# Kernel tuning notes

Hardware: AMD Instinct MI355X
Metric: run time of the kernel (lower is better)

The kernel has to match this reference:

```python
import jax, jax.numpy as jnp
import numpy as np

NUM_HEADS = 8
LN_EPS = 1e-5


def setup_inputs() -> dict:
    key = jax.random.key(0)
    ks = jax.random.split(key, 9)
    B, C, H, W, T = 16, 512, 64, 64, 768
    x = jax.random.normal(ks[0], (B, C, H, W), dtype=jnp.float32)
    text_emb = jax.random.normal(ks[1], (B, T), dtype=jnp.float32)
    # nn.Linear weights are stored (out_features, in_features); y = x @ W.T
    Wq = jax.random.normal(ks[2], (C, C), dtype=jnp.float32) / np.sqrt(C)
    Wk = jax.random.normal(ks[3], (C, T), dtype=jnp.float32) / np.sqrt(T)
    Wv = jax.random.normal(ks[4], (C, T), dtype=jnp.float32) / np.sqrt(T)
    Wo = jax.random.normal(ks[5], (C, C), dtype=jnp.float32) / np.sqrt(C)
    bo = jax.random.normal(ks[6], (C,), dtype=jnp.float32) * 0.02
    gamma = jnp.ones((C,), dtype=jnp.float32)
    beta = jnp.zeros((C,), dtype=jnp.float32)
    return {"x": x, "text_emb": text_emb, "Wq": Wq, "Wk": Wk, "Wv": Wv,
            "Wo": Wo, "bo": bo, "gamma": gamma, "beta": beta}


def _layer_norm(h, gamma, beta):
    mu = jnp.mean(h, axis=-1, keepdims=True)
    var = jnp.mean(jnp.square(h - mu), axis=-1, keepdims=True)
    return (h - mu) * jax.lax.rsqrt(var + LN_EPS) * gamma + beta


def reference(x, text_emb, Wq, Wk, Wv, Wo, bo, gamma, beta):
    B, C, H, W = x.shape
    nh = NUM_HEADS
    hd = C // nh
    S = H * W
    # (B, S, C) spatial-token layout
    xr = x.reshape(B, C, S).transpose(0, 2, 1)
    q = (xr @ Wq.T).reshape(B, S, nh, hd).transpose(0, 2, 1, 3)      # (B, nh, S, hd)
    k = (text_emb @ Wk.T).reshape(B, 1, nh, hd).transpose(0, 2, 1, 3)  # (B, nh, 1, hd)
    v = (text_emb @ Wv.T).reshape(B, 1, nh, hd).transpose(0, 2, 1, 3)  # (B, nh, 1, hd)
    scale = hd ** (-0.5)
    scores = jnp.einsum('bnsh,bnkh->bnsk', q, k) * scale              # (B, nh, S, 1)
    attn = jax.nn.softmax(scores, axis=-1)                            # == 1.0 (single kv)
    out = jnp.einsum('bnsk,bnkh->bnsh', attn, v)                      # (B, nh, S, hd)
    out = out.transpose(0, 2, 1, 3).reshape(B, S, C)
    out = out @ Wo.T + bo
    y = _layer_norm(xr + out, gamma, beta)                            # (B, S, C)
    return y.transpose(0, 2, 1).reshape(B, C, H, W)
```

## Files before the change

### kernel.cpp

```cpp
#include <hip/hip_runtime.h>


constexpr int B = 16, C = 512, T = 768, S = 4096;
constexpr int TS = 32;
constexpr int BLK = 256;
constexpr float LN_EPS = 1e-5f;

template <int K, bool HAS_BIAS>
__global__ __launch_bounds__(256) void gemv_wave(const float* __restrict__ in,
                                                 const float* __restrict__ Wt,
                                                 const float* __restrict__ bias,
                                                 float* __restrict__ out) {
    const int w    = blockIdx.x * 4 + (threadIdx.x >> 6);
    const int lane = threadIdx.x & 63;
    const int b    = w >> 9;
    const int c    = w & (C - 1);
    const float4* wr = reinterpret_cast<const float4*>(Wt + (size_t)c * K);
    const float4* xr = reinterpret_cast<const float4*>(in + (size_t)b * K);
    float acc = 0.f;
#pragma unroll
    for (int i = lane; i < K / 4; i += 64) {
        float4 a = wr[i], t = xr[i];
        acc += a.x * t.x + a.y * t.y + a.z * t.z + a.w * t.w;
    }
#pragma unroll
    for (int off = 32; off > 0; off >>= 1) acc += __shfl_down(acc, off);
    if (lane == 0) out[b * C + c] = HAS_BIAS ? acc + bias[c] : acc;
}

__global__ __launch_bounds__(BLK) void fused_ln(const float* __restrict__ x,
                                                const float* __restrict__ a,
                                                const float* __restrict__ gamma,
                                                const float* __restrict__ beta,
                                                float* __restrict__ out) {
    __shared__ float tile[C * TS];
    __shared__ float a_s[C], g_s[C], be_s[C];
    __shared__ float psum[8 * TS], psq[8 * TS];
    __shared__ float mean_s[TS], rstd_s[TS];

    const int bid = blockIdx.x;
    const int b   = bid >> 7;
    const int s0  = (bid & 127) << 5;
    const int tid = threadIdx.x;

    for (int c = tid; c < C; c += BLK) {
        a_s[c]  = a[b * C + c];
        g_s[c]  = gamma[c];
        be_s[c] = beta[c];
    }

    const float* xb = x + (size_t)b * C * S + s0;
#pragma unroll
    for (int j = 0; j < 16; ++j) {
        int idx = j * BLK + tid;
        int c   = idx >> 3;
        int p   = (idx & 7) << 2;
        float4 v = *reinterpret_cast<const float4*>(xb + (size_t)c * S + p);
        *reinterpret_cast<float4*>(tile + c * TS + p) = v;
    }
    __syncthreads();

    const int w    = tid >> 6;
    const int l    = tid & 63;
    const int s    = l & 31;
    const int sub  = l >> 5;
    const int cbase = w * 128 + sub * 64;

    float sum = 0.f, sq = 0.f;
#pragma unroll 4
    for (int i = 0; i < 64; ++i) {
        int c = cbase + i;
        float v = tile[c * TS + s] + a_s[c];
        sum += v; sq += v * v;
    }
    psum[(w * 2 + sub) * TS + s] = sum;
    psq [(w * 2 + sub) * TS + s] = sq;
    __syncthreads();

    if (tid < TS) {
        float tsum = 0.f, tsq = 0.f;
#pragma unroll
        for (int j = 0; j < 8; ++j) { tsum += psum[j * TS + tid]; tsq += psq[j * TS + tid]; }
        float mu  = tsum * (1.f / C);
        float var = tsq * (1.f / C) - mu * mu;
        mean_s[tid] = mu;
        rstd_s[tid] = rsqrtf(var + LN_EPS);
    }
    __syncthreads();

    float* ob = out + (size_t)b * C * S + s0;
    const float mu = mean_s[s];
    const float rs = rstd_s[s];
#pragma unroll 4
    for (int i = 0; i < 64; ++i) {
        int c = cbase + i;
        float v = tile[c * TS + s] + a_s[c];
        ob[(size_t)c * S + s] = (v - mu) * rs * g_s[c] + be_s[c];
    }
}

extern "C" void kernel_launch(void* const* d_in, const int* in_sizes, int n_in,
                              void* d_out, int out_size, void* d_ws, size_t ws_size,
                              hipStream_t stream) {
    const float* x     = (const float*)d_in[0];
    const float* te    = (const float*)d_in[1];
    const float* Wv    = (const float*)d_in[4];
    const float* Wo    = (const float*)d_in[5];
    const float* bo    = (const float*)d_in[6];
    const float* gamma = (const float*)d_in[7];
    const float* beta  = (const float*)d_in[8];
    float* out = (float*)d_out;
    float* v   = (float*)d_ws;
    float* a   = (float*)d_ws + B * C;

    gemv_wave<T, false><<<B * C / 4, 256, 0, stream>>>(te, Wv, nullptr, v);
    gemv_wave<C, true ><<<B * C / 4, 256, 0, stream>>>(v,  Wo, bo,      a);
    fused_ln<<<B * (S / TS), BLK, 0, stream>>>(x, a, gamma, beta, out);
}
```

Before: 59.08 us.

## Keep LayerNorm tile in registers with float4 column-wise access and shuffle reductions

The fused LayerNorm kernel drops its 64KB shared-memory tile. Each block now covers 16 spatial positions with 512 threads. Every thread holds four float4 values of x in registers, reduces sums across channels with xor shuffles plus a small cross-wave shared-memory step, and writes the result back with vectorized stores. This cuts shared-memory traffic and LDS footprint, which should raise occupancy and allow float4 stores. The cost is short 64-byte contiguous segments per channel row, which may hurt memory coalescing.

```diff
diff --git a/kernel.cpp b/kernel.cpp
--- a/kernel.cpp
+++ b/kernel.cpp
@@ -2,8 +2,6 @@
 
 
 constexpr int B = 16, C = 512, T = 768, S = 4096;
-constexpr int TS = 32;
-constexpr int BLK = 256;
 constexpr float LN_EPS = 1e-5f;
 
 template <int K, bool HAS_BIAS>
@@ -28,74 +26,80 @@
     if (lane == 0) out[b * C + c] = HAS_BIAS ? acc + bias[c] : acc;
 }
 
-__global__ __launch_bounds__(BLK) void fused_ln(const float* __restrict__ x,
+__global__ __launch_bounds__(512) void fused_ln(const float* __restrict__ x,
                                                 const float* __restrict__ a,
                                                 const float* __restrict__ gamma,
                                                 const float* __restrict__ beta,
                                                 float* __restrict__ out) {
-    __shared__ float tile[C * TS];
     __shared__ float a_s[C], g_s[C], be_s[C];
-    __shared__ float psum[8 * TS], psq[8 * TS];
-    __shared__ float mean_s[TS], rstd_s[TS];
+    __shared__ float4 ps[32], pq[32];
 
     const int bid = blockIdx.x;
-    const int b   = bid >> 7;
-    const int s0  = (bid & 127) << 5;
-    const int tid = threadIdx.x;
+    const int b   = bid >> 8;
+    const int s0  = (bid & 255) << 4;
+    const int t   = threadIdx.x;
+    const int s4  = t & 3;
+    const int m   = t >> 2;
 
-    for (int c = tid; c < C; c += BLK) {
-        a_s[c]  = a[b * C + c];
-        g_s[c]  = gamma[c];
-        be_s[c] = beta[c];
+    const float4* xb4 = reinterpret_cast<const float4*>(x + (size_t)b * C * S + s0);
+    float4 xv[4];
+#pragma unroll
+    for (int i = 0; i < 4; ++i)
+        xv[i] = xb4[(size_t)(m + 128 * i) * (S / 4) + s4];
+
+    a_s[t]  = a[b * C + t];
+    g_s[t]  = gamma[t];
+    be_s[t] = beta[t];
+    __syncthreads();
+
+    float4 sum4 = {0.f, 0.f, 0.f, 0.f}, sq4 = {0.f, 0.f, 0.f, 0.f};
+#pragma unroll
+    for (int i = 0; i < 4; ++i) {
+        const float ac = a_s[m + 128 * i];
+        xv[i].x += ac; xv[i].y += ac; xv[i].z += ac; xv[i].w += ac;
+        sum4.x += xv[i].x; sum4.y += xv[i].y; sum4.z += xv[i].z; sum4.w += xv[i].w;
+        sq4.x  += xv[i].x * xv[i].x; sq4.y += xv[i].y * xv[i].y;
+        sq4.z  += xv[i].z * xv[i].z; sq4.w += xv[i].w * xv[i].w;
     }
 
-    const float* xb = x + (size_t)b * C * S + s0;
 #pragma unroll
-    for (int j = 0; j < 16; ++j) {
-        int idx = j * BLK + tid;
-        int c   = idx >> 3;
-        int p   = (idx & 7) << 2;
-        float4 v = *reinterpret_cast<const float4*>(xb + (size_t)c * S + p);
-        *reinterpret_cast<float4*>(tile + c * TS + p) = v;
+    for (int mask = 4; mask <= 32; mask <<= 1) {
+        sum4.x += __shfl_xor(sum4.x, mask); sum4.y += __shfl_xor(sum4.y, mask);
+        sum4.z += __shfl_xor(sum4.z, mask); sum4.w += __shfl_xor(sum4.w, mask);
+        sq4.x  += __shfl_xor(sq4.x,  mask); sq4.y  += __shfl_xor(sq4.y,  mask);
+        sq4.z  += __shfl_xor(sq4.z,  mask); sq4.w  += __shfl_xor(sq4.w,  mask);
     }
+    const int w = t >> 6, l = t & 63;
+    if (l < 4) { ps[w * 4 + l] = sum4; pq[w * 4 + l] = sq4; }
     __syncthreads();
 
-    const int w    = tid >> 6;
-    const int l    = tid & 63;
-    const int s    = l & 31;
-    const int sub  = l >> 5;
-    const int cbase = w * 128 + sub * 64;
+    float4 tot = {0.f, 0.f, 0.f, 0.f}, tq = {0.f, 0.f, 0.f, 0.f};
+#pragma unroll
+    for (int wv = 0; wv < 8; ++wv) {
+        float4 p = ps[wv * 4 + s4];
+        float4 q = pq[wv * 4 + s4];
+        tot.x += p.x; tot.y += p.y; tot.z += p.z; tot.w += p.w;
+        tq.x  += q.x; tq.y  += q.y; tq.z  += q.z; tq.w  += q.w;
+    }
+    constexpr float inv = 1.f / C;
+    float4 mu, rs;
+    mu.x = tot.x * inv; mu.y = tot.y * inv; mu.z = tot.z * inv; mu.w = tot.w * inv;
+    rs.x = rsqrtf(tq.x * inv - mu.x * mu.x + LN_EPS);
+    rs.y = rsqrtf(tq.y * inv - mu.y * mu.y + LN_EPS);
+    rs.z = rsqrtf(tq.z * inv - mu.z * mu.z + LN_EPS);
+    rs.w = rsqrtf(tq.w * inv - mu.w * mu.w + LN_EPS);
 
-    float sum = 0.f, sq = 0.f;
-#pragma unroll 4
-    for (int i = 0; i < 64; ++i) {
-        int c = cbase + i;
-        float v = tile[c * TS + s] + a_s[c];
-        sum += v; sq += v * v;
-    }
-    psum[(w * 2 + sub) * TS + s] = sum;
-    psq [(w * 2 + sub) * TS + s] = sq;
-    __syncthreads();
-
-    if (tid < TS) {
-        float tsum = 0.f, tsq = 0.f;
+    float4* ob4 = reinterpret_cast<float4*>(out + (size_t)b * C * S + s0);
 #pragma unroll
-        for (int j = 0; j < 8; ++j) { tsum += psum[j * TS + tid]; tsq += psq[j * TS + tid]; }
-        float mu  = tsum * (1.f / C);
-        float var = tsq * (1.f / C) - mu * mu;
-        mean_s[tid] = mu;
-        rstd_s[tid] = rsqrtf(var + LN_EPS);
-    }
-    __syncthreads();
-
-    float* ob = out + (size_t)b * C * S + s0;
-    const float mu = mean_s[s];
-    const float rs = rstd_s[s];
-#pragma unroll 4
-    for (int i = 0; i < 64; ++i) {
-        int c = cbase + i;
-        float v = tile[c * TS + s] + a_s[c];
-        ob[(size_t)c * S + s] = (v - mu) * rs * g_s[c] + be_s[c];
+    for (int i = 0; i < 4; ++i) {
+        const int c = m + 128 * i;
+        const float g = g_s[c], be = be_s[c];
+        float4 v = xv[i], o;
+        o.x = (v.x - mu.x) * rs.x * g + be;
+        o.y = (v.y - mu.y) * rs.y * g + be;
+        o.z = (v.z - mu.z) * rs.z * g + be;
+        o.w = (v.w - mu.w) * rs.w * g + be;
+        ob4[(size_t)c * (S / 4) + s4] = o;
     }
 }
 
@@ -115,5 +119,5 @@
 
     gemv_wave<T, false><<<B * C / 4, 256, 0, stream>>>(te, Wv, nullptr, v);
     gemv_wave<C, true ><<<B * C / 4, 256, 0, stream>>>(v,  Wo, bo,      a);
-    fused_ln<<<B * (S / TS), BLK, 0, stream>>>(x, a, gamma, beta, out);
+    fused_ln<<<B * (S / 16), 512, 0, stream>>>(x, a, gamma, beta, out);
 }
```

Measured after the change: 71.52 us. 1.21x slower.
